# Kernel optimization log

Measured on AMD Instinct MI355X. Metric: run time of the kernel, lower is better.

## Reference

```python
import jax, jax.numpy as jnp
import numpy as np

B, H, W, C = 128, 28, 28, 512


def setup_inputs() -> dict:
    key = jax.random.key(0)
    k1, k2 = jax.random.split(key)
    x = jax.random.normal(k1, (B, H, W, C), dtype=jnp.float32)
    t_p = jax.random.uniform(k2, (H, W, H, W), dtype=jnp.float32)
    return {"x": x, "t_p": t_p}


def reference(x, t_p):
    # x: [B,H,W,C] NHWC; t_p: [H,W,H,W] spatial template bank.
    Bx, Hx, Wx, Cx = x.shape
    # Global-spatial max_pool_with_argmax == argmax over flattened H*W per (b,c).
    flat = x.reshape(Bx, Hx * Wx, Cx)
    idx = jnp.argmax(flat, axis=1)            # [B,C] first-max, like TF
    h = idx // Wx                              # [B,C] row of spatial argmax
    w = idx % Wx                               # [B,C] col of spatial argmax
    # Per-(b,c) template gather: t_p[h,w] -> [B,C,H,W]
    templates = t_p[h, w]
    templates = jnp.transpose(templates, (0, 2, 3, 1))  # [B,H,W,C]
    masked = jax.nn.relu(x * templates)
    return masked, x, templates
```

## Files before the change

kernel.cpp:

```cpp
#include <hip/hip_runtime.h>

#define Bn 128
#define Hn 28
#define Wn 28
#define Cn 512
#define Pn (Hn * Wn)
#define SCH 8
#define PCH (Pn / SCH)
#define PPB 56
#define PPT 28

typedef float f4 __attribute__((ext_vector_type(4)));

__device__ __forceinline__ void nt_store4(float* p, float a, float b, float c, float d) {
    f4 v = {a, b, c, d};
    __builtin_nontemporal_store(v, reinterpret_cast<f4*>(p));
}

__global__ void argmax_partial_copy(const float* __restrict__ x,
                                    float* __restrict__ o1,
                                    uint2* __restrict__ part) {
    int s = blockIdx.x & (SCH - 1);
    int b = blockIdx.x >> 3;
    int c0 = threadIdx.x * 4;

    size_t base = (size_t)b * Pn * Cn + c0;
    int p0 = s * PCH;

    float b0 = -INFINITY, b1 = -INFINITY, b2 = -INFINITY, b3 = -INFINITY;
    int i0 = p0, i1 = p0, i2 = p0, i3 = p0;
#pragma unroll 7
    for (int i = 0; i < PCH; ++i) {
        size_t off = base + (size_t)(p0 + i) * Cn;
        float4 v = *reinterpret_cast<const float4*>(x + off);
        nt_store4(o1 + off, v.x, v.y, v.z, v.w);
        if (v.x > b0) { b0 = v.x; i0 = p0 + i; }
        if (v.y > b1) { b1 = v.y; i1 = p0 + i; }
        if (v.z > b2) { b2 = v.z; i2 = p0 + i; }
        if (v.w > b3) { b3 = v.w; i3 = p0 + i; }
    }
    uint2* o = part + (size_t)s * (Bn * Cn) + (size_t)b * Cn + c0;
    o[0] = make_uint2(__float_as_uint(b0), (unsigned)i0);
    o[1] = make_uint2(__float_as_uint(b1), (unsigned)i1);
    o[2] = make_uint2(__float_as_uint(b2), (unsigned)i2);
    o[3] = make_uint2(__float_as_uint(b3), (unsigned)i3);
}

__global__ void argmax_combine(const uint2* __restrict__ part,
                               int* __restrict__ idx) {
    int bc = blockIdx.x * 256 + threadIdx.x;
    float best = -INFINITY;
    int bi = 0;
#pragma unroll
    for (int s = 0; s < SCH; ++s) {
        uint2 r = part[(size_t)s * (Bn * Cn) + bc];
        float v = __uint_as_float(r.x);
        if (v > best) { best = v; bi = (int)r.y; }
    }
    idx[bc] = bi;
}

__global__ void mask_outputs(const float* __restrict__ x,
                             const float* __restrict__ tp,
                             const int* __restrict__ idx,
                             float* __restrict__ o0,
                             float* __restrict__ o2) {
    int pc = blockIdx.x % 14;
    int b  = blockIdx.x / 14;
    int ci = threadIdx.x & 127;
    int c0 = ci * 4;
    int ph = threadIdx.x >> 7;
    int p0 = pc * PPB + ph * PPT;

    int4 iv = *reinterpret_cast<const int4*>(idx + (size_t)b * Cn + c0);
    const float* t0p = tp + (size_t)iv.x * Pn;
    const float* t1p = tp + (size_t)iv.y * Pn;
    const float* t2p = tp + (size_t)iv.z * Pn;
    const float* t3p = tp + (size_t)iv.w * Pn;

    size_t xbase = (size_t)b * Pn * Cn + c0;

#pragma unroll
    for (int j = 0; j < PPT; j += 4) {
        int p = p0 + j;
        float4 ta = *reinterpret_cast<const float4*>(t0p + p);
        float4 tb = *reinterpret_cast<const float4*>(t1p + p);
        float4 tc = *reinterpret_cast<const float4*>(t2p + p);
        float4 td = *reinterpret_cast<const float4*>(t3p + p);
        float4 x0 = *reinterpret_cast<const float4*>(x + xbase + (size_t)(p + 0) * Cn);
        float4 x1 = *reinterpret_cast<const float4*>(x + xbase + (size_t)(p + 1) * Cn);
        float4 x2 = *reinterpret_cast<const float4*>(x + xbase + (size_t)(p + 2) * Cn);
        float4 x3 = *reinterpret_cast<const float4*>(x + xbase + (size_t)(p + 3) * Cn);

        size_t q0 = xbase + (size_t)(p + 0) * Cn;
        size_t q1 = xbase + (size_t)(p + 1) * Cn;
        size_t q2 = xbase + (size_t)(p + 2) * Cn;
        size_t q3 = xbase + (size_t)(p + 3) * Cn;

        nt_store4(o0 + q0, fmaxf(x0.x * ta.x, 0.f), fmaxf(x0.y * tb.x, 0.f),
                           fmaxf(x0.z * tc.x, 0.f), fmaxf(x0.w * td.x, 0.f));
        nt_store4(o0 + q1, fmaxf(x1.x * ta.y, 0.f), fmaxf(x1.y * tb.y, 0.f),
                           fmaxf(x1.z * tc.y, 0.f), fmaxf(x1.w * td.y, 0.f));
        nt_store4(o0 + q2, fmaxf(x2.x * ta.z, 0.f), fmaxf(x2.y * tb.z, 0.f),
                           fmaxf(x2.z * tc.z, 0.f), fmaxf(x2.w * td.z, 0.f));
        nt_store4(o0 + q3, fmaxf(x3.x * ta.w, 0.f), fmaxf(x3.y * tb.w, 0.f),
                           fmaxf(x3.z * tc.w, 0.f), fmaxf(x3.w * td.w, 0.f));
        nt_store4(o2 + q0, ta.x, tb.x, tc.x, td.x);
        nt_store4(o2 + q1, ta.y, tb.y, tc.y, td.y);
        nt_store4(o2 + q2, ta.z, tb.z, tc.z, td.z);
        nt_store4(o2 + q3, ta.w, tb.w, tc.w, td.w);
    }
}

extern "C" void kernel_launch(void* const* d_in, const int* in_sizes, int n_in,
                              void* d_out, int out_size, void* d_ws, size_t ws_size,
                              hipStream_t stream) {
    const float* x  = (const float*)d_in[0];
    const float* tp = (const float*)d_in[1];

    const size_t N = (size_t)Bn * Pn * Cn;
    float* o0 = (float*)d_out;
    float* o1 = o0 + N;
    float* o2 = o0 + 2 * N;

    uint2* part = (uint2*)d_ws;
    int* idx = (int*)((char*)d_ws + (size_t)SCH * Bn * Cn * sizeof(uint2));

    argmax_partial_copy<<<Bn * SCH, 128, 0, stream>>>(x, o1, part);
    argmax_combine<<<(Bn * Cn) / 256, 256, 0, stream>>>(part, idx);
    mask_outputs<<<Bn * 14, 256, 0, stream>>>(x, tp, idx, o0, o2);
}
```

Baseline: 160.6 us.

## Pipeline argmax and masking across batch chunks in one fused kernel

Replaces the three-kernel sequence with nine launches of a single kernel. Each launch computes argmax partials for batch chunk k while combining and masking chunk k-1. The per-chunk combine now lives in the mask blocks and passes indices through shared memory, and the copy of x into the second output moves from the argmax pass to the mask pass. This is meant to keep the chunk's x resident in the large cache between its argmax read and its mask read, so x is streamed from DRAM fewer times. The cost is more launches and a redundant partial combine done by each of the 14 mask blocks per batch.

```diff
diff --git a/kernel.cpp b/kernel.cpp
--- a/kernel.cpp
+++ b/kernel.cpp
@@ -5,8 +5,12 @@
 #define Wn 28
 #define Cn 512
 #define Pn (Hn * Wn)
-#define SCH 8
+#define NCH 8
+#define CB (Bn / NCH)
+#define SCH 28
 #define PCH (Pn / SCH)
+#define ARGB ((CB / 2) * SCH)
+#define MSKB (CB * 14)
 #define PPB 56
 #define PPT 28
 
@@ -16,63 +20,84 @@
     f4 v = {a, b, c, d};
     __builtin_nontemporal_store(v, reinterpret_cast<f4*>(p));
 }
-
-__global__ void argmax_partial_copy(const float* __restrict__ x,
-                                    float* __restrict__ o1,
-                                    uint2* __restrict__ part) {
-    int s = blockIdx.x & (SCH - 1);
-    int b = blockIdx.x >> 3;
-    int c0 = threadIdx.x * 4;
-
-    size_t base = (size_t)b * Pn * Cn + c0;
-    int p0 = s * PCH;
-
-    float b0 = -INFINITY, b1 = -INFINITY, b2 = -INFINITY, b3 = -INFINITY;
-    int i0 = p0, i1 = p0, i2 = p0, i3 = p0;
-#pragma unroll 7
-    for (int i = 0; i < PCH; ++i) {
-        size_t off = base + (size_t)(p0 + i) * Cn;
-        float4 v = *reinterpret_cast<const float4*>(x + off);
-        nt_store4(o1 + off, v.x, v.y, v.z, v.w);
-        if (v.x > b0) { b0 = v.x; i0 = p0 + i; }
-        if (v.y > b1) { b1 = v.y; i1 = p0 + i; }
-        if (v.z > b2) { b2 = v.z; i2 = p0 + i; }
-        if (v.w > b3) { b3 = v.w; i3 = p0 + i; }
-    }
-    uint2* o = part + (size_t)s * (Bn * Cn) + (size_t)b * Cn + c0;
-    o[0] = make_uint2(__float_as_uint(b0), (unsigned)i0);
-    o[1] = make_uint2(__float_as_uint(b1), (unsigned)i1);
-    o[2] = make_uint2(__float_as_uint(b2), (unsigned)i2);
-    o[3] = make_uint2(__float_as_uint(b3), (unsigned)i3);
+__device__ __forceinline__ f4 nt_load4(const float* p) {
+    return __builtin_nontemporal_load(reinterpret_cast<const f4*>(p));
 }
 
-__global__ void argmax_combine(const uint2* __restrict__ part,
-                               int* __restrict__ idx) {
-    int bc = blockIdx.x * 256 + threadIdx.x;
-    float best = -INFINITY;
-    int bi = 0;
+__global__ __launch_bounds__(256) void pipe(const float* __restrict__ x,
+                                            const float* __restrict__ tp,
+                                            float* __restrict__ o0,
+                                            float* __restrict__ o1,
+                                            float* __restrict__ o2,
+                                            uint2* __restrict__ part,
+                                            int k, int nArg) {
+    __shared__ int sidx[Cn];
+
+    if ((int)blockIdx.x < nArg) {
+        int blk = blockIdx.x;
+        int s  = blk % SCH;
+        int bp = blk / SCH;
+        int bl = bp * 2 + (threadIdx.x >> 7);
+        int b  = k * CB + bl;
+        int c0 = (threadIdx.x & 127) * 4;
+
+        size_t base = (size_t)b * Pn * Cn + c0;
+        int p0 = s * PCH;
+
+        float b0 = -INFINITY, b1 = -INFINITY, b2 = -INFINITY, b3 = -INFINITY;
+        int i0 = p0, i1 = p0, i2 = p0, i3 = p0;
+#pragma unroll 7
+        for (int i = 0; i < PCH; ++i) {
+            float4 v = *reinterpret_cast<const float4*>(x + base + (size_t)(p0 + i) * Cn);
+            if (v.x > b0) { b0 = v.x; i0 = p0 + i; }
+            if (v.y > b1) { b1 = v.y; i1 = p0 + i; }
+            if (v.z > b2) { b2 = v.z; i2 = p0 + i; }
+            if (v.w > b3) { b3 = v.w; i3 = p0 + i; }
+        }
+        uint2* o = part + (((size_t)(k & 1) * SCH + s) * CB + bl) * Cn + c0;
+        o[0] = make_uint2(__float_as_uint(b0), (unsigned)i0);
+        o[1] = make_uint2(__float_as_uint(b1), (unsigned)i1);
+        o[2] = make_uint2(__float_as_uint(b2), (unsigned)i2);
+        o[3] = make_uint2(__float_as_uint(b3), (unsigned)i3);
+        return;
+    }
+
+    int blk = blockIdx.x - nArg;
+    int pc = blk % 14;
+    int bl = blk / 14;
+    int b  = (k - 1) * CB + bl;
+    int t  = threadIdx.x;
+
+    if (t < 128) {
+        int c0 = t * 4;
+        const uint2* pp = part + ((size_t)((k - 1) & 1) * SCH * CB + bl) * Cn + c0;
+        float v0 = -INFINITY, v1 = -INFINITY, v2 = -INFINITY, v3 = -INFINITY;
+        int j0 = 0, j1 = 0, j2 = 0, j3 = 0;
 #pragma unroll
-    for (int s = 0; s < SCH; ++s) {
-        uint2 r = part[(size_t)s * (Bn * Cn) + bc];
-        float v = __uint_as_float(r.x);
-        if (v > best) { best = v; bi = (int)r.y; }
+        for (int s = 0; s < SCH; ++s) {
+            const uint2* q = pp + (size_t)s * (CB * Cn);
+            uint4 a = *reinterpret_cast<const uint4*>(q);
+            uint4 c = *reinterpret_cast<const uint4*>(q + 2);
+            float f0 = __uint_as_float(a.x), f1 = __uint_as_float(a.z);
+            float f2 = __uint_as_float(c.x), f3 = __uint_as_float(c.z);
+            if (f0 > v0) { v0 = f0; j0 = (int)a.y; }
+            if (f1 > v1) { v1 = f1; j1 = (int)a.w; }
+            if (f2 > v2) { v2 = f2; j2 = (int)c.y; }
+            if (f3 > v3) { v3 = f3; j3 = (int)c.w; }
+        }
+        sidx[c0 + 0] = j0;
+        sidx[c0 + 1] = j1;
+        sidx[c0 + 2] = j2;
+        sidx[c0 + 3] = j3;
     }
-    idx[bc] = bi;
-}
+    __syncthreads();
 
-__global__ void mask_outputs(const float* __restrict__ x,
-                             const float* __restrict__ tp,
-                             const int* __restrict__ idx,
-                             float* __restrict__ o0,
-                             float* __restrict__ o2) {
-    int pc = blockIdx.x % 14;
-    int b  = blockIdx.x / 14;
-    int ci = threadIdx.x & 127;
+    int ci = t & 127;
     int c0 = ci * 4;
-    int ph = threadIdx.x >> 7;
+    int ph = t >> 7;
     int p0 = pc * PPB + ph * PPT;
 
-    int4 iv = *reinterpret_cast<const int4*>(idx + (size_t)b * Cn + c0);
+    int4 iv = *reinterpret_cast<const int4*>(sidx + c0);
     const float* t0p = tp + (size_t)iv.x * Pn;
     const float* t1p = tp + (size_t)iv.y * Pn;
     const float* t2p = tp + (size_t)iv.z * Pn;
@@ -87,16 +112,20 @@
         float4 tb = *reinterpret_cast<const float4*>(t1p + p);
         float4 tc = *reinterpret_cast<const float4*>(t2p + p);
         float4 td = *reinterpret_cast<const float4*>(t3p + p);
-        float4 x0 = *reinterpret_cast<const float4*>(x + xbase + (size_t)(p + 0) * Cn);
-        float4 x1 = *reinterpret_cast<const float4*>(x + xbase + (size_t)(p + 1) * Cn);
-        float4 x2 = *reinterpret_cast<const float4*>(x + xbase + (size_t)(p + 2) * Cn);
-        float4 x3 = *reinterpret_cast<const float4*>(x + xbase + (size_t)(p + 3) * Cn);
+        f4 x0 = nt_load4(x + xbase + (size_t)(p + 0) * Cn);
+        f4 x1 = nt_load4(x + xbase + (size_t)(p + 1) * Cn);
+        f4 x2 = nt_load4(x + xbase + (size_t)(p + 2) * Cn);
+        f4 x3 = nt_load4(x + xbase + (size_t)(p + 3) * Cn);
 
         size_t q0 = xbase + (size_t)(p + 0) * Cn;
         size_t q1 = xbase + (size_t)(p + 1) * Cn;
         size_t q2 = xbase + (size_t)(p + 2) * Cn;
         size_t q3 = xbase + (size_t)(p + 3) * Cn;
 
+        nt_store4(o1 + q0, x0.x, x0.y, x0.z, x0.w);
+        nt_store4(o1 + q1, x1.x, x1.y, x1.z, x1.w);
+        nt_store4(o1 + q2, x2.x, x2.y, x2.z, x2.w);
+        nt_store4(o1 + q3, x3.x, x3.y, x3.z, x3.w);
         nt_store4(o0 + q0, fmaxf(x0.x * ta.x, 0.f), fmaxf(x0.y * tb.x, 0.f),
                            fmaxf(x0.z * tc.x, 0.f), fmaxf(x0.w * td.x, 0.f));
         nt_store4(o0 + q1, fmaxf(x1.x * ta.y, 0.f), fmaxf(x1.y * tb.y, 0.f),
@@ -124,9 +153,10 @@
     float* o2 = o0 + 2 * N;
 
     uint2* part = (uint2*)d_ws;
-    int* idx = (int*)((char*)d_ws + (size_t)SCH * Bn * Cn * sizeof(uint2));
 
-    argmax_partial_copy<<<Bn * SCH, 128, 0, stream>>>(x, o1, part);
-    argmax_combine<<<(Bn * Cn) / 256, 256, 0, stream>>>(part, idx);
-    mask_outputs<<<Bn * 14, 256, 0, stream>>>(x, tp, idx, o0, o2);
+    for (int k = 0; k <= NCH; ++k) {
+        int nArg  = (k < NCH) ? ARGB : 0;
+        int nMask = (k > 0) ? MSKB : 0;
+        pipe<<<nArg + nMask, 256, 0, stream>>>(x, tp, o0, o1, o2, part, k, nArg);
+    }
 }
```

Result: slower. 195.7 us (+21.9%).
